# Optimization experiments

Measured on AMD Instinct MI355X. Metric: run time of the kernel, lower is better.

## Reference

```python
import jax, jax.numpy as jnp
import numpy as np

TANH_CONST = 1.5  # tanh_constant in __init__
EPS = 1e-9


def setup_inputs() -> dict:
    key = jax.random.key(0)
    ks = jax.random.split(key, 6)
    B, H, NOPS, T = 8192, 100, 5, 512
    return {
        "x0": jax.random.uniform(ks[0], (B, H), dtype=jnp.float32),          # g_emb-style uniform start input
        "W_x": jax.random.normal(ks[1], (H, 4 * H), dtype=jnp.float32) * 0.1,  # LSTMCell kernel (no bias)
        "W_h": jax.random.normal(ks[2], (H, 4 * H), dtype=jnp.float32) * 0.1,  # LSTMCell recurrent kernel
        "W_ops": jax.random.normal(ks[3], (H, NOPS), dtype=jnp.float32) * 0.1, # dense_ops (no bias)
        "emb": jax.random.normal(ks[4], (NOPS + 1, H), dtype=jnp.float32),     # Embedding(num_ops+1, lstm_size)
        "u": jax.random.uniform(ks[5], (T, B, NOPS), dtype=jnp.float32),       # uniform noise -> Gumbel-max sampling
    }


def reference(x0, W_x, W_h, W_ops, emb, u):
    # Gumbel noise for categorical sampling (equiv. in distribution to tf.random.categorical)
    g = -jnp.log(-jnp.log(u + EPS) + EPS)  # [T, B, num_ops]
    B, H = x0.shape

    def step(carry, g_t):
        h, c, x = carry
        # Keras LSTMCell, use_bias=False: gate order (i, f, c, o)
        z = x @ W_x + h @ W_h                      # [B, 4H]
        zi, zf, zc, zo = jnp.split(z, 4, axis=-1)
        c_new = jax.nn.sigmoid(zf) * c + jax.nn.sigmoid(zi) * jnp.tanh(zc)
        h_new = jax.nn.sigmoid(zo) * jnp.tanh(c_new)
        logits = TANH_CONST * jnp.tanh(h_new @ W_ops)  # tanh_constant * tanh(dense_ops(h))
        op = jnp.argmax(logits + g_t, axis=-1)         # [B] sampled op ids
        logp = jax.nn.log_softmax(logits, axis=-1)
        cur = -jnp.take_along_axis(logp, op[:, None], axis=-1)[:, 0]  # sparse xent vs sampled label
        ent = jax.lax.stop_gradient(cur * jnp.exp(-cur))
        x_new = emb[op]                                # next-step input = embedding(op_id)
        return (h_new, c_new, x_new), (cur, ent, op)

    h0 = jnp.zeros((B, H), x0.dtype)
    c0 = jnp.zeros((B, H), x0.dtype)
    _, (curs, ents, ops) = jax.lax.scan(step, (h0, c0, x0), g)
    log_prob = curs.sum(0)   # [B] accumulated self.log_prob
    entropy = ents.sum(0)    # [B] accumulated self.entropy
    return log_prob, entropy, ops
```

## Files before the change

### kernel.cpp

```cpp
#include <hip/hip_runtime.h>
#include <cstdint>
#include <cstddef>

typedef __attribute__((ext_vector_type(8))) short short8;
typedef __attribute__((ext_vector_type(4))) short bfx4;
typedef __attribute__((ext_vector_type(4))) float f32x4;

#define HH     100
#define G4     400
#define NCOL   416
#define NTIL   26
#define KTN    3
#define KRES   96
#define BTOT   8192
#define TST    512
#define ROWS   32
#define NBLK   256
#define BLOCK  832
#define ZW     420
#define TANHC  1.5f
#define EPSF   1e-9f

__device__ unsigned short d_Bhi[NTIL*KTN*64*8];
__device__ unsigned short d_Blo[NTIL*KTN*64*8];
__device__ float d_Ep2[6*G4];
__device__ float d_WresG[NCOL*4];
__device__ float d_Z0[(size_t)BTOT*G4];

static __device__ __forceinline__ unsigned short bf16hi(float f){
  unsigned u = __float_as_uint(f);
  return (unsigned short)((u + 0x7FFFu + ((u>>16)&1u)) >> 16);
}
static __device__ __forceinline__ float bf16f(unsigned short s){
  return __uint_as_float(((unsigned)s)<<16);
}
static __device__ __forceinline__ float frcp(float x){ return __builtin_amdgcn_rcpf(x); }
static __device__ __forceinline__ float sigf(float x){ return frcp(1.0f + __expf(-x)); }
static __device__ __forceinline__ float tanh_f(float x){ return 1.0f - 2.0f*frcp(__expf(2.0f*x) + 1.0f); }


__global__ void setup_bpack(const float* __restrict__ Wh, const float* __restrict__ Wops){
  int idx = blockIdx.x*blockDim.x + threadIdx.x;
  if (idx >= NTIL*KTN*64) return;
  int tile = idx/(KTN*64), rem = idx - tile*(KTN*64), kt = rem>>6, ln = rem&63;
  int n = tile*16 + (ln & 15);
  #pragma unroll
  for (int i = 0; i < 8; ++i){
    int k = kt*32 + (ln>>4)*8 + i;
    float w = 0.f;
    if (n < G4)          w = Wh[k*G4 + n];
    else if (n < G4+5)   w = Wops[k*5 + (n - G4)];
    unsigned short hi = bf16hi(w);
    unsigned short lo = bf16hi(w - bf16f(hi));
    d_Bhi[idx*8+i] = hi;
    d_Blo[idx*8+i] = lo;
  }
}

__global__ void setup_misc(const float* __restrict__ emb, const float* __restrict__ Wx,
                           const float* __restrict__ Wh, const float* __restrict__ Wops){
  int idx = blockIdx.x*blockDim.x + threadIdx.x;
  if (idx < 6*G4){
    int e = idx/G4, r2 = idx - e*G4, je = r2>>2, g = r2&3;
    float s = 0.f;
    for (int k = 0; k < HH; ++k) s = fmaf(emb[e*HH+k], Wx[k*G4 + g*HH + je], s);
    d_Ep2[idx] = s;
  } else if (idx < 6*G4 + NCOL*4){
    int i = idx - 6*G4, n = i>>2, q = i&3;
    float w = 0.f;
    if (n < G4)        w = Wh[(KRES+q)*G4 + n];
    else if (n < G4+5) w = Wops[(KRES+q)*5 + (n - G4)];
    d_WresG[i] = w;
  }
}

__global__ __launch_bounds__(256) void setup_z0(const float* __restrict__ x0,
                                                const float* __restrict__ Wx){
  __shared__ float xs[64*101];
  const int bb = blockIdx.x * 64;
  for (int i = threadIdx.x; i < 64*HH; i += 256){
    int r = i/HH, k = i - r*HH;
    xs[r*101 + k] = x0[(size_t)(bb + r)*HH + k];
  }
  __syncthreads();
  const int bl = threadIdx.x & 63;
  for (int ng = threadIdx.x >> 6; ng < HH; ng += 4){
    f32x4 a = {0.f,0.f,0.f,0.f};
    for (int k = 0; k < HH; ++k){
      f32x4 w = *(const f32x4*)&Wx[k*G4 + ng*4];
      a += w * xs[bl*101 + k];
    }
    *(f32x4*)&d_Z0[(size_t)(bb + bl)*G4 + ng*4] = a;
  }
}


__global__ __launch_bounds__(BLOCK) void rnn_main(
    const float* __restrict__ u, float* __restrict__ out)
{
  __shared__ __align__(16) float z_lds[ROWS*ZW];
  __shared__ __align__(16) unsigned short fhi[2*KTN*64*8];
  __shared__ __align__(16) unsigned short flo[2*KTN*64*8];
  __shared__ __align__(16) float h_res[4*ROWS];
  __shared__ __align__(16) float Ep2_l[6*G4];
  __shared__ __align__(16) float Wres_l[NCOL*4];
  __shared__ __align__(16) float samp[5*36];
  __shared__ __align__(16) float gn_lds[ROWS*5];
  __shared__ int op_lds[ROWS];

  const int tid  = threadIdx.x;
  const int wave = tid >> 6;
  const int lane = tid & 63;
  const int cn   = lane & 15;
  const int q4   = lane >> 4;
  const int row0 = blockIdx.x * ROWS;
  const int jg   = tid >> 5;
  const int rE   = tid & 31;

  for (int i = tid; i < 6*G4;   i += BLOCK) Ep2_l[i]  = d_Ep2[i];
  for (int i = tid; i < NCOL*4; i += BLOCK) Wres_l[i] = d_WresG[i];

  short8 bh[2][KTN], bl[2][KTN];
  {
    const short8* bph = (const short8*)d_Bhi;
    const short8* bpl = (const short8*)d_Blo;
    #pragma unroll
    for (int tl = 0; tl < 2; ++tl)
      #pragma unroll
      for (int kt = 0; kt < KTN; ++kt){
        int fi = ((wave*2 + tl)*KTN + kt)*64 + lane;
        bh[tl][kt] = bph[fi];
        bl[tl][kt] = bpl[fi];
      }
  }

  float c_st[4] = {0.f,0.f,0.f,0.f};
  float lp_acc = 0.f, ent_acc = 0.f;

  for (int t = 0; t <= TST; ++t){
    if (t == 0){
      if (tid < 800){
        #pragma unroll
        for (int i = 0; i < 4; ++i){
          f32x4 v = *(const f32x4*)&d_Z0[(size_t)(row0 + rE)*G4 + jg*16 + i*4];
          *(f32x4*)&z_lds[rE*ZW + jg*16 + i*4] = v;
        }
      }
    } else {
      #pragma unroll
      for (int mt = 0; mt < 2; ++mt){
        short8 ah[KTN], al[KTN];
        #pragma unroll
        for (int kt = 0; kt < KTN; ++kt){
          ah[kt] = *(const short8*)&fhi[((mt*KTN + kt)*64 + lane)*8];
          al[kt] = *(const short8*)&flo[((mt*KTN + kt)*64 + lane)*8];
        }
        f32x4 hq[4];
        #pragma unroll
        for (int q = 0; q < 4; ++q)
          hq[q] = *(const f32x4*)&h_res[q*ROWS + mt*16 + q4*4];
        #pragma unroll
        for (int tl = 0; tl < 2; ++tl){
          const int n = (wave*2 + tl)*16 + cn;
          f32x4 acc = {0.f,0.f,0.f,0.f};
          #pragma unroll
          for (int kt = 0; kt < KTN; ++kt){
            acc = __builtin_amdgcn_mfma_f32_16x16x32_bf16(ah[kt], bh[tl][kt], acc, 0,0,0);
            acc = __builtin_amdgcn_mfma_f32_16x16x32_bf16(al[kt], bh[tl][kt], acc, 0,0,0);
            acc = __builtin_amdgcn_mfma_f32_16x16x32_bf16(ah[kt], bl[tl][kt], acc, 0,0,0);
            acc = __builtin_amdgcn_mfma_f32_16x16x32_bf16(al[kt], bl[tl][kt], acc, 0,0,0);
          }
          f32x4 wr = *(const f32x4*)&Wres_l[n*4];
          #pragma unroll
          for (int q = 0; q < 4; ++q) acc += hq[q] * wr[q];
          const int rowb = mt*16 + q4*4;
          #pragma unroll
          for (int i = 0; i < 4; ++i)
            z_lds[(rowb + i)*ZW + n] = acc[i];
          if (wave == 12 && tl == 1 && cn < 5)
            *(f32x4*)&samp[cn*36 + mt*16 + q4*4] = acc;
        }
      }
      if (wave == 12 && lane < 32){
        int r = lane;
        float l[5];
        #pragma unroll
        for (int o = 0; o < 5; ++o) l[o] = TANHC * tanh_f(samp[o*36 + r]);
        int op = 0; float best = -1e30f;
        #pragma unroll
        for (int o = 0; o < 5; ++o){
          float v = l[o] + gn_lds[r*5 + o];
          if (v > best){ best = v; op = o; }
        }
        float mx = fmaxf(fmaxf(fmaxf(l[0],l[1]), fmaxf(l[2],l[3])), l[4]);
        float se = 0.f;
        #pragma unroll
        for (int o = 0; o < 5; ++o) se += __expf(l[o] - mx);
        float lse = mx + __logf(se);
        float cur = lse - l[op];
        lp_acc  += cur;
        ent_acc += cur * __expf(-cur);
        op_lds[r] = op;
        out[2*BTOT + (size_t)(t-1)*BTOT + row0 + r] = (float)op;
      }
    }
    if (t == TST) break;
    __syncthreads();

    if (tid < 800){
      f32x4 zg[4];
      #pragma unroll
      for (int g = 0; g < 4; ++g)
        zg[g] = *(const f32x4*)&z_lds[rE*ZW + g*HH + jg*4];
      if (t > 0){
        const int op = op_lds[rE];
        #pragma unroll
        for (int i = 0; i < 4; ++i){
          f32x4 e4 = *(const f32x4*)&Ep2_l[op*G4 + (jg*4 + i)*4];
          zg[0][i] += e4.x; zg[1][i] += e4.y; zg[2][i] += e4.z; zg[3][i] += e4.w;
        }
      }
      float hv[4];
      #pragma unroll
      for (int i = 0; i < 4; ++i){
        float cn_ = sigf(zg[1][i])*c_st[i] + sigf(zg[0][i])*tanh_f(zg[2][i]);
        c_st[i] = cn_;
        hv[i] = sigf(zg[3][i])*tanh_f(cn_);
      }
      if (jg < 24){
        bfx4 h4, l4;
        #pragma unroll
        for (int i = 0; i < 4; ++i){
          unsigned short hi = bf16hi(hv[i]);
          h4[i] = (short)hi;
          l4[i] = (short)bf16hi(hv[i] - bf16f(hi));
        }
        const int kt   = jg >> 3;
        const int lf   = (rE & 15) | (((jg >> 1) & 3) << 4);
        const int mt   = rE >> 4;
        const int j0   = (jg & 1) * 4;
        const int base = ((mt*KTN + kt)*64 + lf)*8 + j0;
        *(bfx4*)&fhi[base] = h4;
        *(bfx4*)&flo[base] = l4;
      } else {
        #pragma unroll
        for (int i = 0; i < 4; ++i) h_res[i*ROWS + rE] = hv[i];
      }
    } else {
      int r = tid - 800;
      const float* up = u + ((size_t)t*BTOT + row0 + r)*5;
      #pragma unroll
      for (int o = 0; o < 5; ++o){
        float uu = up[o];
        gn_lds[r*5 + o] = -__logf(-__logf(uu + EPSF) + EPSF);
      }
    }
    __syncthreads();
  }

  if (wave == 12 && lane < 32){
    out[row0 + lane]        = lp_acc;
    out[BTOT + row0 + lane] = ent_acc;
  }
}

extern "C" void kernel_launch(void* const* d_in, const int* in_sizes, int n_in,
                              void* d_out, int out_size, void* d_ws, size_t ws_size,
                              hipStream_t stream) {
  const float* x0   = (const float*)d_in[0];
  const float* Wx   = (const float*)d_in[1];
  const float* Wh   = (const float*)d_in[2];
  const float* Wops = (const float*)d_in[3];
  const float* emb  = (const float*)d_in[4];
  const float* u    = (const float*)d_in[5];
  (void)d_ws; (void)ws_size; (void)in_sizes; (void)n_in;

  setup_bpack<<<(NTIL*KTN*64 + 255)/256, 256, 0, stream>>>(Wh, Wops);
  setup_misc<<<(6*G4 + NCOL*4 + 255)/256, 256, 0, stream>>>(emb, Wx, Wh, Wops);
  setup_z0<<<BTOT/64, 256, 0, stream>>>(x0, Wx);
  rnn_main<<<NBLK, BLOCK, 0, stream>>>(u, (float*)d_out);
}
```

Measured before the change: 2.273 ms.

## Split block rows into two half-groups and interleave matmul with gate phases

Each block's 32 rows become two groups of 16 with separate LDS buffers. Within one barrier interval, the MFMA matmul for one group runs alongside the elementwise LSTM gate update for the other, so the two phases overlap instead of strictly alternating. The split-bf16 product also drops the lo*lo MFMA term, going from four passes to three and slightly reducing precision. Barriers per timestep stay at two, but each phase now works on half the rows.

```diff
diff --git a/kernel.cpp b/kernel.cpp
--- a/kernel.cpp
+++ b/kernel.cpp
@@ -3,7 +3,7 @@
 #include <cstddef>
 
 typedef __attribute__((ext_vector_type(8))) short short8;
-typedef __attribute__((ext_vector_type(4))) short bfx4;
+typedef __attribute__((ext_vector_type(2))) float f32x2;
 typedef __attribute__((ext_vector_type(4))) float f32x4;
 
 #define HH     100
@@ -15,6 +15,7 @@
 #define BTOT   8192
 #define TST    512
 #define ROWS   32
+#define HALF   16
 #define NBLK   256
 #define BLOCK  832
 #define ZW     420
@@ -98,15 +99,15 @@
 __global__ __launch_bounds__(BLOCK) void rnn_main(
     const float* __restrict__ u, float* __restrict__ out)
 {
-  __shared__ __align__(16) float z_lds[ROWS*ZW];
-  __shared__ __align__(16) unsigned short fhi[2*KTN*64*8];
-  __shared__ __align__(16) unsigned short flo[2*KTN*64*8];
-  __shared__ __align__(16) float h_res[4*ROWS];
+  __shared__ __align__(16) float z_l[2][HALF*ZW];
+  __shared__ __align__(16) unsigned short fhi_l[2][KTN*64*8];
+  __shared__ __align__(16) unsigned short flo_l[2][KTN*64*8];
+  __shared__ __align__(16) float hres_l[2][4*HALF];
   __shared__ __align__(16) float Ep2_l[6*G4];
   __shared__ __align__(16) float Wres_l[NCOL*4];
-  __shared__ __align__(16) float samp[5*36];
-  __shared__ __align__(16) float gn_lds[ROWS*5];
-  __shared__ int op_lds[ROWS];
+  __shared__ __align__(16) float samp[5*20];
+  __shared__ __align__(16) float gn_l[2][HALF*5];
+  __shared__ int op_l[2][HALF];
 
   const int tid  = threadIdx.x;
   const int wave = tid >> 6;
@@ -114,8 +115,9 @@
   const int cn   = lane & 15;
   const int q4   = lane >> 4;
   const int row0 = blockIdx.x * ROWS;
-  const int jg   = tid >> 5;
-  const int rE   = tid & 31;
+  const int jg2  = tid >> 4;
+  const int rE   = tid & 15;
+  const int j0   = jg2 * 2;
 
   for (int i = tid; i < 6*G4;   i += BLOCK) Ep2_l[i]  = d_Ep2[i];
   for (int i = tid; i < NCOL*4; i += BLOCK) Wres_l[i] = d_WresG[i];
@@ -134,133 +136,134 @@
       }
   }
 
-  float c_st[4] = {0.f,0.f,0.f,0.f};
-  float lp_acc = 0.f, ent_acc = 0.f;
-
-  for (int t = 0; t <= TST; ++t){
-    if (t == 0){
-      if (tid < 800){
-        #pragma unroll
-        for (int i = 0; i < 4; ++i){
-          f32x4 v = *(const f32x4*)&d_Z0[(size_t)(row0 + rE)*G4 + jg*16 + i*4];
-          *(f32x4*)&z_lds[rE*ZW + jg*16 + i*4] = v;
-        }
-      }
-    } else {
-      #pragma unroll
-      for (int mt = 0; mt < 2; ++mt){
-        short8 ah[KTN], al[KTN];
-        #pragma unroll
-        for (int kt = 0; kt < KTN; ++kt){
-          ah[kt] = *(const short8*)&fhi[((mt*KTN + kt)*64 + lane)*8];
-          al[kt] = *(const short8*)&flo[((mt*KTN + kt)*64 + lane)*8];
-        }
-        f32x4 hq[4];
-        #pragma unroll
-        for (int q = 0; q < 4; ++q)
-          hq[q] = *(const f32x4*)&h_res[q*ROWS + mt*16 + q4*4];
-        #pragma unroll
-        for (int tl = 0; tl < 2; ++tl){
-          const int n = (wave*2 + tl)*16 + cn;
-          f32x4 acc = {0.f,0.f,0.f,0.f};
-          #pragma unroll
-          for (int kt = 0; kt < KTN; ++kt){
-            acc = __builtin_amdgcn_mfma_f32_16x16x32_bf16(ah[kt], bh[tl][kt], acc, 0,0,0);
-            acc = __builtin_amdgcn_mfma_f32_16x16x32_bf16(al[kt], bh[tl][kt], acc, 0,0,0);
-            acc = __builtin_amdgcn_mfma_f32_16x16x32_bf16(ah[kt], bl[tl][kt], acc, 0,0,0);
-            acc = __builtin_amdgcn_mfma_f32_16x16x32_bf16(al[kt], bl[tl][kt], acc, 0,0,0);
-          }
-          f32x4 wr = *(const f32x4*)&Wres_l[n*4];
-          #pragma unroll
-          for (int q = 0; q < 4; ++q) acc += hq[q] * wr[q];
-          const int rowb = mt*16 + q4*4;
-          #pragma unroll
-          for (int i = 0; i < 4; ++i)
-            z_lds[(rowb + i)*ZW + n] = acc[i];
-          if (wave == 12 && tl == 1 && cn < 5)
-            *(f32x4*)&samp[cn*36 + mt*16 + q4*4] = acc;
-        }
-      }
-      if (wave == 12 && lane < 32){
-        int r = lane;
-        float l[5];
-        #pragma unroll
-        for (int o = 0; o < 5; ++o) l[o] = TANHC * tanh_f(samp[o*36 + r]);
-        int op = 0; float best = -1e30f;
-        #pragma unroll
-        for (int o = 0; o < 5; ++o){
-          float v = l[o] + gn_lds[r*5 + o];
-          if (v > best){ best = v; op = o; }
-        }
-        float mx = fmaxf(fmaxf(fmaxf(l[0],l[1]), fmaxf(l[2],l[3])), l[4]);
-        float se = 0.f;
-        #pragma unroll
-        for (int o = 0; o < 5; ++o) se += __expf(l[o] - mx);
-        float lse = mx + __logf(se);
-        float cur = lse - l[op];
-        lp_acc  += cur;
-        ent_acc += cur * __expf(-cur);
-        op_lds[r] = op;
-        out[2*BTOT + (size_t)(t-1)*BTOT + row0 + r] = (float)op;
-      }
-    }
+  float c_st[2][2] = {{0.f,0.f},{0.f,0.f}};
+  float lp_acc[2]  = {0.f,0.f};
+  float ent_acc[2] = {0.f,0.f};
+
+#define RUN_SEGMENT(GG, EG, TE_EXPR)                                          \
+  {                                                                           \
+    const int tE = (TE_EXPR);                                                 \
+    if (t == 0){                                                              \
+      if (tid < 800){                                                         \
+        _Pragma("unroll")                                                     \
+        for (int ii = 0; ii < 2; ++ii){                                       \
+          f32x4 v = *(const f32x4*)&d_Z0[(size_t)(row0 + GG*HALF + rE)*G4 + jg2*8 + ii*4]; \
+          *(f32x4*)&z_l[GG][rE*ZW + jg2*8 + ii*4] = v;                        \
+        }                                                                     \
+      }                                                                       \
+    } else {                                                                  \
+      short8 ah[KTN], al[KTN];                                                \
+      _Pragma("unroll")                                                       \
+      for (int kt = 0; kt < KTN; ++kt){                                       \
+        ah[kt] = *(const short8*)&fhi_l[GG][(kt*64 + lane)*8];                \
+        al[kt] = *(const short8*)&flo_l[GG][(kt*64 + lane)*8];                \
+      }                                                                       \
+      _Pragma("unroll")                                                       \
+      for (int tl = 0; tl < 2; ++tl){                                         \
+        const int n = (wave*2 + tl)*16 + cn;                                  \
+        f32x4 acc = {0.f,0.f,0.f,0.f};                                        \
+        _Pragma("unroll")                                                     \
+        for (int kt = 0; kt < KTN; ++kt){                                     \
+          acc = __builtin_amdgcn_mfma_f32_16x16x32_bf16(ah[kt], bh[tl][kt], acc, 0,0,0); \
+          acc = __builtin_amdgcn_mfma_f32_16x16x32_bf16(al[kt], bh[tl][kt], acc, 0,0,0); \
+          acc = __builtin_amdgcn_mfma_f32_16x16x32_bf16(ah[kt], bl[tl][kt], acc, 0,0,0); \
+        }                                                                     \
+        f32x4 wr = *(const f32x4*)&Wres_l[n*4];                               \
+        _Pragma("unroll")                                                     \
+        for (int q = 0; q < 4; ++q){                                          \
+          f32x4 hq = *(const f32x4*)&hres_l[GG][q*HALF + q4*4];               \
+          acc += hq * wr[q];                                                  \
+        }                                                                     \
+        if (t < TST){                                                         \
+          _Pragma("unroll")                                                   \
+          for (int i = 0; i < 4; ++i)                                         \
+            z_l[GG][(q4*4 + i)*ZW + n] = acc[i];                              \
+        }                                                                     \
+        if (wave == 12 && tl == 1 && cn < 5)                                  \
+          *(f32x4*)&samp[cn*20 + q4*4] = acc;                                 \
+      }                                                                       \
+      if (wave == 12 && lane < HALF){                                         \
+        const int r = lane;                                                   \
+        float l[5];                                                           \
+        _Pragma("unroll")                                                     \
+        for (int o = 0; o < 5; ++o) l[o] = TANHC * tanh_f(samp[o*20 + r]);    \
+        int op = 0; float best = -1e30f;                                      \
+        _Pragma("unroll")                                                     \
+        for (int o = 0; o < 5; ++o){                                          \
+          float v = l[o] + gn_l[GG][r*5 + o];                                 \
+          if (v > best){ best = v; op = o; }                                  \
+        }                                                                     \
+        float mx = fmaxf(fmaxf(fmaxf(l[0],l[1]), fmaxf(l[2],l[3])), l[4]);    \
+        float se = 0.f;                                                       \
+        _Pragma("unroll")                                                     \
+        for (int o = 0; o < 5; ++o) se += __expf(l[o] - mx);                  \
+        float lse = mx + __logf(se);                                          \
+        float cur = lse - l[op];                                              \
+        lp_acc[GG]  += cur;                                                   \
+        ent_acc[GG] += cur * __expf(-cur);                                    \
+        op_l[GG][r] = op;                                                     \
+        out[2*BTOT + (size_t)(t-1)*BTOT + row0 + GG*HALF + r] = (float)op;    \
+      }                                                                       \
+    }                                                                         \
+    if (tE >= 0 && tE < TST){                                                 \
+      if (tid < 800){                                                         \
+        f32x2 zg[4];                                                          \
+        _Pragma("unroll")                                                     \
+        for (int gg = 0; gg < 4; ++gg)                                        \
+          zg[gg] = *(const f32x2*)&z_l[EG][rE*ZW + gg*HH + j0];               \
+        if (tE > 0){                                                          \
+          const int op = op_l[EG][rE];                                        \
+          f32x4 e0 = *(const f32x4*)&Ep2_l[op*G4 + j0*4];                     \
+          f32x4 e1 = *(const f32x4*)&Ep2_l[op*G4 + (j0+1)*4];                 \
+          zg[0][0] += e0.x; zg[1][0] += e0.y; zg[2][0] += e0.z; zg[3][0] += e0.w; \
+          zg[0][1] += e1.x; zg[1][1] += e1.y; zg[2][1] += e1.z; zg[3][1] += e1.w; \
+        }                                                                     \
+        float hv[2];                                                          \
+        _Pragma("unroll")                                                     \
+        for (int i = 0; i < 2; ++i){                                          \
+          float cc = sigf(zg[1][i])*c_st[EG][i] + sigf(zg[0][i])*tanh_f(zg[2][i]); \
+          c_st[EG][i] = cc;                                                   \
+          hv[i] = sigf(zg[3][i])*tanh_f(cc);                                  \
+        }                                                                     \
+        if (j0 < KRES){                                                       \
+          unsigned short h0 = bf16hi(hv[0]), h1 = bf16hi(hv[1]);              \
+          unsigned short lo0 = bf16hi(hv[0] - bf16f(h0));                     \
+          unsigned short lo1 = bf16hi(hv[1] - bf16f(h1));                     \
+          const int kt = j0 >> 5;                                             \
+          const int lf = rE + (((j0 >> 3) & 3) << 4);                         \
+          const int hw = (kt*64 + lf)*8 + (j0 & 7);                           \
+          *(unsigned*)&fhi_l[EG][hw] = (unsigned)h0  | ((unsigned)h1  << 16); \
+          *(unsigned*)&flo_l[EG][hw] = (unsigned)lo0 | ((unsigned)lo1 << 16); \
+        } else {                                                              \
+          hres_l[EG][(j0 - KRES)*HALF + rE]     = hv[0];                      \
+          hres_l[EG][(j0 - KRES + 1)*HALF + rE] = hv[1];                      \
+        }                                                                     \
+      } else if (tid < 816){                                                  \
+        const int r = tid - 800;                                              \
+        const float* up = u + ((size_t)tE*BTOT + row0 + EG*HALF + r)*5;       \
+        _Pragma("unroll")                                                     \
+        for (int o = 0; o < 5; ++o){                                          \
+          float uu = up[o];                                                   \
+          gn_l[EG][r*5 + o] = -__logf(-__logf(uu + EPSF) + EPSF);             \
+        }                                                                     \
+      }                                                                       \
+    }                                                                         \
+  }
+
+  for (int t = 0; ; ++t){
+    RUN_SEGMENT(0, 1, t-1)
+    __syncthreads();
+    RUN_SEGMENT(1, 0, t)
     if (t == TST) break;
     __syncthreads();
-
-    if (tid < 800){
-      f32x4 zg[4];
-      #pragma unroll
-      for (int g = 0; g < 4; ++g)
-        zg[g] = *(const f32x4*)&z_lds[rE*ZW + g*HH + jg*4];
-      if (t > 0){
-        const int op = op_lds[rE];
-        #pragma unroll
-        for (int i = 0; i < 4; ++i){
-          f32x4 e4 = *(const f32x4*)&Ep2_l[op*G4 + (jg*4 + i)*4];
-          zg[0][i] += e4.x; zg[1][i] += e4.y; zg[2][i] += e4.z; zg[3][i] += e4.w;
-        }
-      }
-      float hv[4];
-      #pragma unroll
-      for (int i = 0; i < 4; ++i){
-        float cn_ = sigf(zg[1][i])*c_st[i] + sigf(zg[0][i])*tanh_f(zg[2][i]);
-        c_st[i] = cn_;
-        hv[i] = sigf(zg[3][i])*tanh_f(cn_);
-      }
-      if (jg < 24){
-        bfx4 h4, l4;
-        #pragma unroll
-        for (int i = 0; i < 4; ++i){
-          unsigned short hi = bf16hi(hv[i]);
-          h4[i] = (short)hi;
-          l4[i] = (short)bf16hi(hv[i] - bf16f(hi));
-        }
-        const int kt   = jg >> 3;
-        const int lf   = (rE & 15) | (((jg >> 1) & 3) << 4);
-        const int mt   = rE >> 4;
-        const int j0   = (jg & 1) * 4;
-        const int base = ((mt*KTN + kt)*64 + lf)*8 + j0;
-        *(bfx4*)&fhi[base] = h4;
-        *(bfx4*)&flo[base] = l4;
-      } else {
-        #pragma unroll
-        for (int i = 0; i < 4; ++i) h_res[i*ROWS + rE] = hv[i];
-      }
-    } else {
-      int r = tid - 800;
-      const float* up = u + ((size_t)t*BTOT + row0 + r)*5;
-      #pragma unroll
-      for (int o = 0; o < 5; ++o){
-        float uu = up[o];
-        gn_lds[r*5 + o] = -__logf(-__logf(uu + EPSF) + EPSF);
-      }
-    }
-    __syncthreads();
-  }
-
-  if (wave == 12 && lane < 32){
-    out[row0 + lane]        = lp_acc;
-    out[BTOT + row0 + lane] = ent_acc;
+  }
+#undef RUN_SEGMENT
+
+  if (wave == 12 && lane < HALF){
+    out[row0 + lane]               = lp_acc[0];
+    out[row0 + HALF + lane]        = lp_acc[1];
+    out[BTOT + row0 + lane]        = ent_acc[0];
+    out[BTOT + row0 + HALF + lane] = ent_acc[1];
   }
 }
 
```

Measured after the change: 2.804 ms. +23.4%, slower.
